# Performance work log

Measured on AMD Instinct MI355X. Metric: run time of the kernel, lower is better.

Reference implementation:

```python
import jax, jax.numpy as jnp
import numpy as np

B, M, H, NH, D, L = 4, 1024, 1024, 8, 128, 1024
E, TOPK, F = 8, 2, 4096
MU, GAMMA = 0.7, 1.0


def _skew(X):
    # shift every row one step right: [B, M, L] -> [B, M, M+L]
    b, m, l = X.shape
    X = jnp.pad(X, ((0, 0), (0, 0), (0, m + 1)))
    X = X.reshape(b, -1)[:, :-m]
    return X.reshape(b, m, m + l)


def _unskew(X):
    # reverse of _skew: [B, M, M+L] -> [B, M, L] (banded diagonal extraction)
    b, m, lt = X.shape
    l = lt - m
    X = jnp.pad(X.reshape(b, -1), ((0, 0), (0, m)))
    X = X.reshape(b, m, m + l + 1)
    return X[:, :, :l]


def _layernorm(x, g, bta):
    mu = jnp.mean(x, axis=-1, keepdims=True)
    var = jnp.mean(jnp.square(x - mu), axis=-1, keepdims=True)
    return (x - mu) * jax.lax.rsqrt(var + 1e-5) * g + bta


def setup_inputs() -> dict:
    key = jax.random.key(0)
    ks = jax.random.split(key, 12)
    s = 0.02
    return {
        'h': jax.random.normal(ks[0], (B, M, H), jnp.float32),
        'h_cache': jax.random.normal(ks[1], (B, L, H), jnp.float32),
        'pos_encoding': jax.random.normal(ks[2], (1, D, L), jnp.float32) * s,
        'momentum': jnp.zeros((B, M, H), jnp.float32),
        'Wq': jax.random.normal(ks[3], (H, H), jnp.float32) * s,
        'Wk': jax.random.normal(ks[4], (H, H), jnp.float32) * s,
        'Wv': jax.random.normal(ks[5], (H, H), jnp.float32) * s,
        'Wo': jax.random.normal(ks[6], (H, H), jnp.float32) * s,
        'gate_w': jax.random.normal(ks[7], (H, E), jnp.float32) * s,
        'gate_b': jnp.zeros((E,), jnp.float32),
        'w1': jax.random.normal(ks[8], (E, H, F), jnp.float32) * s,
        'b1': jnp.zeros((E, F), jnp.float32),
        'w2': jax.random.normal(ks[9], (E, F, H), jnp.float32) * s,
        'b2': jnp.zeros((E, H), jnp.float32),
        'ln1_g': jnp.ones((H,), jnp.float32),
        'ln1_b': jnp.zeros((H,), jnp.float32),
        'ln2_g': jnp.ones((H,), jnp.float32),
        'ln2_b': jnp.zeros((H,), jnp.float32),
    }


def _heads(x):
    b, n, _ = x.shape
    return x.reshape(b, n, NH, D).transpose(0, 2, 1, 3).reshape(b * NH, n, D)


def reference(h, h_cache, pos_encoding, momentum, Wq, Wk, Wv, Wo,
              gate_w, gate_b, w1, b1, w2, b2, ln1_g, ln1_b, ln2_g, ln2_b):
    b, m, hs = h.shape
    # ---- banded relative-position attention (skew trick) ----
    h_all = jnp.concatenate([h_cache, h], axis=1)            # [B, L+M, H]
    q = _heads(h @ Wq)                                        # [B*K, M, D]
    k = _heads(h_all @ Wk)                                    # [B*K, L+M, D]
    v = _heads(h_all @ Wv)                                    # [B*K, L+M, D]
    ctx = jnp.einsum('bmd,bnd->bmn', q, k)                    # [B*K, M, M+L]
    ctx = _unskew(ctx)                                        # [B*K, M, L]
    pos = jnp.einsum('bmd,dl->bml', q, pos_encoding[0])       # [B*K, M, L]
    attn = jax.nn.softmax((ctx + pos) / np.sqrt(hs), axis=-1)
    attn = _skew(attn)                                        # [B*K, M, M+L]
    out = jnp.einsum('bmn,bnd->bmd', attn, v)                 # [B*K, M, D]
    out = out.reshape(b, NH, m, D).transpose(0, 2, 1, 3).reshape(b, m, hs)
    h1 = _layernorm(h + out @ Wo, ln1_g, ln1_b)
    # ---- MoE (naive balanced top-k gate) + momentum residual ----
    x = h1.reshape(-1, hs)                                    # [N, H]
    logits = x @ gate_w + gate_b                              # [N, E]
    topv, topi = jax.lax.top_k(logits, TOPK)
    wgt = jax.nn.softmax(topv, axis=-1)
    dense = jnp.zeros_like(logits).at[jnp.arange(x.shape[0])[:, None], topi].set(wgt)
    moe = jnp.zeros_like(x)
    for e in range(E):
        ye = jax.nn.relu(x @ w1[e] + b1[e]) @ w2[e] + b2[e]
        moe = moe + dense[:, e:e + 1] * ye
    moe = moe.reshape(b, m, hs)
    mom_new = MU * momentum + GAMMA * moe
    h2 = _layernorm(h1 - mom_new, ln2_g, ln2_b)
    return h2, mom_new
```

## Files before the change

### kernel.cpp

```cpp
#include <hip/hip_runtime.h>


typedef short short8 __attribute__((ext_vector_type(8)));
typedef float f32x4 __attribute__((ext_vector_type(4)));

typedef const void __attribute__((address_space(1)))* gas1_t;
typedef void __attribute__((address_space(3)))* las3_t;
#define ASYNC16(G, L) __builtin_amdgcn_global_load_lds((gas1_t)(G), (las3_t)(L), 16, 0, 0)

#define DEV __device__ __forceinline__

DEV float bf2f(unsigned short u) {
  union { unsigned int u; float f; } x; x.u = ((unsigned int)u) << 16; return x.f;
}
DEV unsigned short f2bf(float f) {
  union { float f; unsigned int u; } x; x.f = f;
  unsigned int r = x.u + 0x7fffu + ((x.u >> 16) & 1u);
  return (unsigned short)(r >> 16);
}

struct GemmP {
  const unsigned short* Ah; const unsigned short* Al;
  const unsigned short* Bh; const unsigned short* Bl;
  void* C; void* C2;
  const float* bias;
  const float* xtra;
  const int* idx; const int2* tmap; const int* tn;
  long a_zo, a_zi;
  long b_zo, b_zi, b_y;
  long c_zo, c_zi, c_y, c_x;
  long x_zo, x_zi, x_y;
  long bias_z;
  int lda, ldb, ldc, xld;
  int K, Kc, nx, zdiv, mode, split;
};

template <int SPLIT>
__global__ __launch_bounds__(256) void kGemm(GemmP p) {
  const int t = threadIdx.x;
  const int bx = blockIdx.x, by = blockIdx.y, bz = blockIdx.z;
  const int zo = bz / p.zdiv, zi = bz % p.zdiv;
  const int bxn = bx % p.nx, kc = bx / p.nx;

  long aOff = 0, bOff, cOff;
  long ar0, ar1;
  int e = zi;
  if (p.tmap) {
    if (by >= *p.tn) return;
    int2 tm = p.tmap[by];
    e = tm.x;
    long base = tm.y;
    cOff = base * p.ldc + (long)bxn * p.c_x;
    bOff = (long)e * p.b_zi + (long)bxn * 128L * p.ldb;
    if (p.idx) { ar0 = p.idx[base + (t >> 2)]; ar1 = p.idx[base + 64 + (t >> 2)]; }
    else { ar0 = base + (t >> 2); ar1 = ar0 + 64; }
  } else {
    aOff = (long)zo * p.a_zo + (long)zi * p.a_zi;
    bOff = (long)zo * p.b_zo + (long)zi * p.b_zi + (long)by * p.b_y + (long)bxn * 128L * p.ldb;
    cOff = (long)zo * p.c_zo + (long)zi * p.c_zi + (long)by * p.c_y + (long)bxn * p.c_x;
    ar0 = by * 128 + (t >> 2); ar1 = ar0 + 64;
  }

  const int scol = (((t & 3) ^ ((t >> 3) & 3)) << 3);
  const unsigned short* A0h = p.Ah + aOff + ar0 * (long)p.lda + scol;
  const unsigned short* A1h = p.Ah + aOff + ar1 * (long)p.lda + scol;
  const unsigned short* B0h = p.Bh + bOff + (long)(t >> 2) * p.ldb + scol;
  const unsigned short* B1h = B0h + 64L * p.ldb;
  const unsigned short *A0l = nullptr, *A1l = nullptr, *B0l = nullptr, *B1l = nullptr;
  if (SPLIT) {
    A0l = p.Al + aOff + ar0 * (long)p.lda + scol;
    A1l = p.Al + aOff + ar1 * (long)p.lda + scol;
    B0l = p.Bl + bOff + (long)(t >> 2) * p.ldb + scol;
    B1l = B0l + 64L * p.ldb;
  }

  const int wave = t >> 6;
  const int lane = t & 63;
  const int quad = lane >> 4, l15 = lane & 15;
  const int wr = (wave >> 1) * 64, wc = (wave & 1) * 64;
  const int qs = ((quad ^ ((l15 >> 1) & 3)) << 3);

  f32x4 acc[4][4] = {};
  const int kt0 = (kc * p.Kc) >> 5;
  const int ktN = kt0 + (p.Kc >> 5);

  if constexpr (SPLIT) {
    __shared__ short sAh[4096], sAl[4096], sBh[4096], sBl[4096];
    for (int kt = kt0; kt < ktN; ++kt) {
      const int k0 = kt << 5;
      ASYNC16(A0h + k0, &sAh[wave * 512]);
      ASYNC16(A1h + k0, &sAh[2048 + wave * 512]);
      ASYNC16(B0h + k0, &sBh[wave * 512]);
      ASYNC16(B1h + k0, &sBh[2048 + wave * 512]);
      ASYNC16(A0l + k0, &sAl[wave * 512]);
      ASYNC16(A1l + k0, &sAl[2048 + wave * 512]);
      ASYNC16(B0l + k0, &sBl[wave * 512]);
      ASYNC16(B1l + k0, &sBl[2048 + wave * 512]);
      __syncthreads();
      short8 fa[4], fb[4];
#pragma unroll
      for (int i = 0; i < 4; ++i) {
        fa[i] = *(const short8*)&sAh[(wr + i * 16 + l15) * 32 + qs];
        fb[i] = *(const short8*)&sBh[(wc + i * 16 + l15) * 32 + qs];
      }
#pragma unroll
      for (int bi = 0; bi < 4; ++bi)
#pragma unroll
        for (int bj = 0; bj < 4; ++bj)
          acc[bi][bj] = __builtin_amdgcn_mfma_f32_16x16x32_bf16(fa[bi], fb[bj], acc[bi][bj], 0, 0, 0);
      {
        short8 ga[4], gb[4];
#pragma unroll
        for (int i = 0; i < 4; ++i) {
          ga[i] = *(const short8*)&sAl[(wr + i * 16 + l15) * 32 + qs];
          gb[i] = *(const short8*)&sBl[(wc + i * 16 + l15) * 32 + qs];
        }
#pragma unroll
        for (int bi = 0; bi < 4; ++bi)
#pragma unroll
          for (int bj = 0; bj < 4; ++bj) {
            acc[bi][bj] = __builtin_amdgcn_mfma_f32_16x16x32_bf16(fa[bi], gb[bj], acc[bi][bj], 0, 0, 0);
            acc[bi][bj] = __builtin_amdgcn_mfma_f32_16x16x32_bf16(ga[bi], fb[bj], acc[bi][bj], 0, 0, 0);
          }
      }
      __syncthreads();
    }
  } else {
    __shared__ short sA[2][4096], sB[2][4096];
    int cur = 0;
    {
      const int k0 = kt0 << 5;
      ASYNC16(A0h + k0, &sA[0][wave * 512]);
      ASYNC16(A1h + k0, &sA[0][2048 + wave * 512]);
      ASYNC16(B0h + k0, &sB[0][wave * 512]);
      ASYNC16(B1h + k0, &sB[0][2048 + wave * 512]);
    }
    for (int kt = kt0; kt < ktN; ++kt) {
      if (kt + 1 < ktN) {
        const int k1 = (kt + 1) << 5;
        ASYNC16(A0h + k1, &sA[cur ^ 1][wave * 512]);
        ASYNC16(A1h + k1, &sA[cur ^ 1][2048 + wave * 512]);
        ASYNC16(B0h + k1, &sB[cur ^ 1][wave * 512]);
        ASYNC16(B1h + k1, &sB[cur ^ 1][2048 + wave * 512]);
        asm volatile("s_waitcnt vmcnt(4)" ::: "memory");
      } else {
        asm volatile("s_waitcnt vmcnt(0)" ::: "memory");
      }
      __builtin_amdgcn_s_barrier();
      short8 fa[4], fb[4];
#pragma unroll
      for (int i = 0; i < 4; ++i) {
        fa[i] = *(const short8*)&sA[cur][(wr + i * 16 + l15) * 32 + qs];
        fb[i] = *(const short8*)&sB[cur][(wc + i * 16 + l15) * 32 + qs];
      }
#pragma unroll
      for (int bi = 0; bi < 4; ++bi)
#pragma unroll
        for (int bj = 0; bj < 4; ++bj)
          acc[bi][bj] = __builtin_amdgcn_mfma_f32_16x16x32_bf16(fa[bi], fb[bj], acc[bi][bj], 0, 0, 0);
      __builtin_amdgcn_s_barrier();
      cur ^= 1;
    }
  }

  long xOff = 0;
  if (p.mode == 3) xOff = (long)zo * p.x_zo + (long)zi * p.x_zi + (long)by * p.x_y;
#pragma unroll
  for (int bj = 0; bj < 4; ++bj) {
    const int n_loc = wc + bj * 16 + l15;
    float bv = 0.0f;
    if (p.bias) bv = p.bias[(long)e * p.bias_z + (long)bxn * 128 + n_loc];
#pragma unroll
    for (int bi = 0; bi < 4; ++bi) {
#pragma unroll
      for (int r = 0; r < 4; ++r) {
        const int m_loc = wr + bi * 16 + quad * 4 + r;
        float v = acc[bi][bj][r];
        if (p.mode == 0) {
          ((float*)p.C)[cOff + (long)m_loc * p.ldc + n_loc] = v + bv;
        } else if (p.mode == 1) {
          long a = cOff + (long)m_loc * p.ldc + n_loc;
          unsigned short hv = f2bf(v);
          ((unsigned short*)p.C)[a] = hv;
          ((unsigned short*)p.C2)[a] = f2bf(v - bf2f(hv));
        } else if (p.mode == 2) {
          long a = cOff + (long)n_loc * p.ldc + m_loc;
          unsigned short hv = f2bf(v);
          ((unsigned short*)p.C)[a] = hv;
          ((unsigned short*)p.C2)[a] = f2bf(v - bf2f(hv));
        } else if (p.mode == 3) {
          int l = bxn * 128 + n_loc - m_loc;
          float outv;
          if ((unsigned)l < 1024u)
            outv = (v + p.xtra[xOff + (long)m_loc * p.xld + l]) * 0.03125f;
          else
            outv = -1e30f;
          ((float*)p.C)[cOff + (long)m_loc * p.ldc + n_loc] = outv;
        } else if (p.mode == 4) {
          float rv = v + bv;
          rv = rv > 0.0f ? rv : 0.0f;
          ((unsigned short*)p.C)[cOff + (long)m_loc * p.ldc + n_loc] = f2bf(rv);
        } else {
          float av = v + (kc == 0 ? bv : 0.0f);
          atomicAdd(&((float*)p.C)[cOff + (long)m_loc * p.ldc + n_loc], av);
        }
      }
    }
  }
}

__global__ __launch_bounds__(256) void kConcatSplit(const float* __restrict__ h,
                                                    const float* __restrict__ hc,
                                                    unsigned short* __restrict__ Xh,
                                                    unsigned short* __restrict__ Xl) {
  long i = (((long)blockIdx.x) * 256 + threadIdx.x) * 4;
  long b = i >> 21;
  long rem = i & 2097151;
  const float* s = (rem < 1048576) ? (hc + b * 1048576 + rem) : (h + b * 1048576 + (rem - 1048576));
  f32x4 v = *(const f32x4*)s;
#pragma unroll
  for (int j = 0; j < 4; ++j) {
    float x = v[j];
    unsigned short hi = f2bf(x);
    Xh[i + j] = hi;
    Xl[i + j] = f2bf(x - bf2f(hi));
  }
}

__global__ __launch_bounds__(256) void kTransposeSplit(const float* __restrict__ src, long src_z,
                                                       int R, int C,
                                                       unsigned short* __restrict__ dh,
                                                       unsigned short* __restrict__ dl, long dst_z) {
  __shared__ float tile[32][33];
  const int z = blockIdx.z;
  const float* s = src + (long)z * src_z;
  const int c0 = blockIdx.x * 32, r0 = blockIdx.y * 32;
  const int tx = threadIdx.x & 31, ty = threadIdx.x >> 5;
  for (int i = 0; i < 32; i += 8)
    tile[ty + i][tx] = s[(long)(r0 + ty + i) * C + c0 + tx];
  __syncthreads();
  unsigned short* ph = dh + (long)z * dst_z;
  for (int i = 0; i < 32; i += 8) {
    int c = c0 + ty + i;
    float v = tile[tx][ty + i];
    unsigned short hv = f2bf(v);
    ph[(long)c * R + r0 + tx] = hv;
    if (dl) dl[(long)z * dst_z + (long)c * R + r0 + tx] = f2bf(v - bf2f(hv));
  }
}

__global__ __launch_bounds__(256) void kSplitF(const float* __restrict__ src,
                                               unsigned short* __restrict__ hi,
                                               unsigned short* __restrict__ lo, int n4) {
  int i = blockIdx.x * 256 + threadIdx.x;
  if (i >= n4) return;
  f32x4 v = ((const f32x4*)src)[i];
#pragma unroll
  for (int j = 0; j < 4; ++j) {
    float x = v[j];
    unsigned short h = f2bf(x);
    hi[i * 4 + j] = h;
    lo[i * 4 + j] = f2bf(x - bf2f(h));
  }
}

__global__ __launch_bounds__(256) void kSoftmax(const float* __restrict__ S,
                                                unsigned short* __restrict__ Ph,
                                                unsigned short* __restrict__ Pl) {
  __shared__ float red[4];
  const long r = blockIdx.x;
  const float* s = S + r * 1152;
  const int t = threadIdx.x;
  float v[5];
  float mx = -3e38f;
#pragma unroll
  for (int i = 0; i < 5; ++i) {
    int c = t + i * 256;
    v[i] = (c < 1152) ? s[c] : -3e38f;
    mx = fmaxf(mx, v[i]);
  }
  for (int o = 32; o; o >>= 1) mx = fmaxf(mx, __shfl_xor(mx, o));
  if ((t & 63) == 0) red[t >> 6] = mx;
  __syncthreads();
  mx = fmaxf(fmaxf(red[0], red[1]), fmaxf(red[2], red[3]));
  __syncthreads();
  float e[5]; float sum = 0.f;
#pragma unroll
  for (int i = 0; i < 5; ++i) {
    int c = t + i * 256;
    e[i] = (c < 1152) ? expf(v[i] - mx) : 0.f;
    sum += e[i];
  }
  for (int o = 32; o; o >>= 1) sum += __shfl_xor(sum, o);
  if ((t & 63) == 0) red[t >> 6] = sum;
  __syncthreads();
  sum = red[0] + red[1] + red[2] + red[3];
  const float inv = 1.0f / sum;
#pragma unroll
  for (int i = 0; i < 5; ++i) {
    int c = t + i * 256;
    if (c < 1152) {
      float pv = e[i] * inv;
      unsigned short hv = f2bf(pv);
      Ph[r * 1152 + c] = hv;
      Pl[r * 1152 + c] = f2bf(pv - bf2f(hv));
    }
  }
}

DEV float blockReduceSum(float v, float* red) {
  for (int o = 32; o; o >>= 1) v += __shfl_xor(v, o);
  if ((threadIdx.x & 63) == 0) red[threadIdx.x >> 6] = v;
  __syncthreads();
  v = red[0] + red[1] + red[2] + red[3];
  __syncthreads();
  return v;
}

__global__ __launch_bounds__(256) void kLN1(const float* __restrict__ h, const float* __restrict__ aw,
                                            const float* __restrict__ g, const float* __restrict__ b,
                                            float* __restrict__ h1f, unsigned short* __restrict__ h1h) {
  __shared__ float red[4];
  const long r = blockIdx.x;
  const int t = threadIdx.x;
  float x[4]; float s = 0.f;
#pragma unroll
  for (int i = 0; i < 4; ++i) { int c = t + i * 256; x[i] = h[r * 1024 + c] + aw[r * 1024 + c]; s += x[i]; }
  float mu = blockReduceSum(s, red) * (1.0f / 1024.0f);
  float q = 0.f;
#pragma unroll
  for (int i = 0; i < 4; ++i) { float d = x[i] - mu; q += d * d; }
  float var = blockReduceSum(q, red) * (1.0f / 1024.0f);
  float rstd = 1.0f / sqrtf(var + 1e-5f);
#pragma unroll
  for (int i = 0; i < 4; ++i) {
    int c = t + i * 256;
    float y = (x[i] - mu) * rstd * g[c] + b[c];
    h1f[r * 1024 + c] = y;
    h1h[r * 1024 + c] = f2bf(y);
  }
}

__global__ __launch_bounds__(256) void kLN2(const float* __restrict__ h1f, const float* __restrict__ mom,
                                            const float* __restrict__ g, const float* __restrict__ b,
                                            float* __restrict__ out) {
  __shared__ float red[4];
  const long r = blockIdx.x;
  const int t = threadIdx.x;
  float x[4]; float s = 0.f;
#pragma unroll
  for (int i = 0; i < 4; ++i) { int c = t + i * 256; x[i] = h1f[r * 1024 + c] - mom[r * 1024 + c]; s += x[i]; }
  float mu = blockReduceSum(s, red) * (1.0f / 1024.0f);
  float q = 0.f;
#pragma unroll
  for (int i = 0; i < 4; ++i) { float d = x[i] - mu; q += d * d; }
  float var = blockReduceSum(q, red) * (1.0f / 1024.0f);
  float rstd = 1.0f / sqrtf(var + 1e-5f);
#pragma unroll
  for (int i = 0; i < 4; ++i) {
    int c = t + i * 256;
    out[r * 1024 + c] = (x[i] - mu) * rstd * g[c] + b[c];
  }
}

__global__ __launch_bounds__(256) void kGate(const float* __restrict__ h1f, const float* __restrict__ gw,
                                             const float* __restrict__ gb,
                                             int2* __restrict__ sel, float2* __restrict__ wgt) {
  const int w = threadIdx.x >> 6, lane = threadIdx.x & 63;
  const long r = (long)blockIdx.x * 4 + w;
  float acc[8] = {0, 0, 0, 0, 0, 0, 0, 0};
  const float* xr = h1f + r * 1024;
  for (int kk = lane; kk < 1024; kk += 64) {
    float x = xr[kk];
    const float* gg = gw + kk * 8;
#pragma unroll
    for (int e = 0; e < 8; ++e) acc[e] += x * gg[e];
  }
#pragma unroll
  for (int e = 0; e < 8; ++e)
    for (int o = 32; o; o >>= 1) acc[e] += __shfl_xor(acc[e], o);
  if (lane == 0) {
    float lg[8];
#pragma unroll
    for (int e = 0; e < 8; ++e) lg[e] = acc[e] + gb[e];
    int e0 = 0; float v0 = lg[0];
#pragma unroll
    for (int e = 1; e < 8; ++e) if (lg[e] > v0) { v0 = lg[e]; e0 = e; }
    int e1 = -1; float v1 = -3e38f;
#pragma unroll
    for (int e = 0; e < 8; ++e) if (e != e0 && lg[e] > v1) { v1 = lg[e]; e1 = e; }
    float ed = expf(v1 - v0);
    float si = 1.0f / (1.0f + ed);
    sel[r] = make_int2(e0, e1);
    wgt[r] = make_float2(si, ed * si);
  }
}

__global__ void kCount(const int2* __restrict__ sel, int* __restrict__ cnt) {
  int r = blockIdx.x * 256 + threadIdx.x;
  if (r < 4096) { int2 s = sel[r]; atomicAdd(&cnt[s.x], 1); atomicAdd(&cnt[s.y], 1); }
}
__global__ void kScan(const int* __restrict__ cnt, int* __restrict__ off,
                      int2* __restrict__ tmap, int* __restrict__ tn) {
  if (threadIdx.x == 0) {
    int run = 0, nt = 0;
    for (int e = 0; e < 8; ++e) {
      off[e] = run;
      int nb = (cnt[e] + 127) >> 7;
      for (int j = 0; j < nb; ++j) { tmap[nt] = make_int2(e, run + (j << 7)); ++nt; }
      run += nb << 7;
    }
    *tn = nt;
  }
}
__global__ void kScatter(const int2* __restrict__ sel, const int* __restrict__ off,
                         int* __restrict__ cur, int* __restrict__ bucket, int2* __restrict__ slotof) {
  int r = blockIdx.x * 256 + threadIdx.x;
  if (r < 4096) {
    int2 s = sel[r];
    int a0 = off[s.x] + atomicAdd(&cur[s.x], 1);
    int a1 = off[s.y] + atomicAdd(&cur[s.y], 1);
    bucket[a0] = r; bucket[a1] = r;
    slotof[r] = make_int2(a0, a1);
  }
}

__global__ __launch_bounds__(256) void kCombine(const float* __restrict__ Z, const int2* __restrict__ slotof,
                                                const float2* __restrict__ wgt, const float* __restrict__ mom_in,
                                                float* __restrict__ mom_out) {
  const long r = blockIdx.x;
  const int t = threadIdx.x;
  int2 sl = slotof[r];
  float2 w = wgt[r];
  const float* z0 = Z + (long)sl.x * 1024;
  const float* z1 = Z + (long)sl.y * 1024;
#pragma unroll
  for (int i = 0; i < 4; ++i) {
    int c = t + i * 256;
    float moe = w.x * z0[c] + w.y * z1[c];
    mom_out[r * 1024 + c] = 0.7f * mom_in[r * 1024 + c] + moe;
  }
}

extern "C" void kernel_launch(void* const* d_in, const int* in_sizes, int n_in,
                              void* d_out, int out_size, void* d_ws, size_t ws_size,
                              hipStream_t stream) {
  (void)in_sizes; (void)n_in; (void)out_size; (void)ws_size;
  const float* h       = (const float*)d_in[0];
  const float* h_cache = (const float*)d_in[1];
  const float* pos     = (const float*)d_in[2];
  const float* mom_in  = (const float*)d_in[3];
  const float* Wq      = (const float*)d_in[4];
  const float* Wk      = (const float*)d_in[5];
  const float* Wv      = (const float*)d_in[6];
  const float* Wo      = (const float*)d_in[7];
  const float* gate_w  = (const float*)d_in[8];
  const float* gate_b  = (const float*)d_in[9];
  const float* w1      = (const float*)d_in[10];
  const float* b1      = (const float*)d_in[11];
  const float* w2      = (const float*)d_in[12];
  const float* b2      = (const float*)d_in[13];
  const float* ln1g    = (const float*)d_in[14];
  const float* ln1b    = (const float*)d_in[15];
  const float* ln2g    = (const float*)d_in[16];
  const float* ln2b    = (const float*)d_in[17];
  float* out = (float*)d_out;

  char* ws = (char*)d_ws;
  float*          S     = (float*)(ws + 0L);
  unsigned short* Y1    = (unsigned short*)(ws + 0L);
  unsigned short* Oh    = (unsigned short*)(ws + 0L);
  unsigned short* Ol    = (unsigned short*)(ws + 8388608L);
  float*          Ppos  = (float*)(ws + 75497472L);
  unsigned short* w1T   = (unsigned short*)(ws + 75497472L);
  unsigned short* Ph    = (unsigned short*)(ws + 142606336L);
  unsigned short* Pl    = (unsigned short*)(ws + 180355072L);
  unsigned short* w2T   = (unsigned short*)(ws + 142606336L);
  unsigned short* Xh    = (unsigned short*)(ws + 218103808L);
  unsigned short* Xl    = (unsigned short*)(ws + 234881024L);
  float*          attnO = (float*)(ws + 218103808L);
  float*          attnWo= (float*)(ws + 234881024L);
  unsigned short* kh    = (unsigned short*)(ws + 251658240L);
  unsigned short* kl    = (unsigned short*)(ws + 268435456L);
  float*          h1f   = (float*)(ws + 251658240L);
  unsigned short* h1h   = (unsigned short*)(ws + 268435456L);
  unsigned short* VTh   = (unsigned short*)(ws + 285212672L);
  unsigned short* VTl   = (unsigned short*)(ws + 301989888L);
  unsigned short* qh    = (unsigned short*)(ws + 318767104L);
  unsigned short* ql    = (unsigned short*)(ws + 327155712L);
  float*          qtmp  = (float*)(ws + 335544320L);
  float*          Z     = (float*)(ws + 335544320L);
  unsigned short* WqTh  = (unsigned short*)(ws + 373293056L);
  unsigned short* WqTl  = (unsigned short*)(ws + 375390208L);
  unsigned short* WkTh  = (unsigned short*)(ws + 377487360L);
  unsigned short* WkTl  = (unsigned short*)(ws + 379584512L);
  unsigned short* WvTh  = (unsigned short*)(ws + 381681664L);
  unsigned short* WvTl  = (unsigned short*)(ws + 383778816L);
  unsigned short* WoTh  = (unsigned short*)(ws + 385875968L);
  unsigned short* WoTl  = (unsigned short*)(ws + 387973120L);
  unsigned short* posTh = (unsigned short*)(ws + 390070272L);
  unsigned short* posTl = (unsigned short*)(ws + 390332416L);
  int2*           sel   = (int2*)(ws + 390594560L);
  float2*         wgt   = (float2*)(ws + 390627328L);
  int2*           slotof= (int2*)(ws + 390660096L);
  int*            bucket= (int*)(ws + 390692864L);
  int*            cnt   = (int*)(ws + 390729728L);
  int*            cur   = (int*)(ws + 390729760L);
  int*            off   = (int*)(ws + 390729792L);
  int2*           tmap  = (int2*)(ws + 390729856L);
  int*            tn    = (int*)(ws + 390730496L);

  kConcatSplit<<<8192, 256, 0, stream>>>(h, h_cache, Xh, Xl);
  kTransposeSplit<<<dim3(32, 32, 1), 256, 0, stream>>>(Wq, 0, 1024, 1024, WqTh, WqTl, 0);
  kTransposeSplit<<<dim3(32, 32, 1), 256, 0, stream>>>(Wk, 0, 1024, 1024, WkTh, WkTl, 0);
  kTransposeSplit<<<dim3(32, 32, 1), 256, 0, stream>>>(Wv, 0, 1024, 1024, WvTh, WvTl, 0);
  kTransposeSplit<<<dim3(32, 32, 1), 256, 0, stream>>>(Wo, 0, 1024, 1024, WoTh, WoTl, 0);
  kTransposeSplit<<<dim3(32, 4, 1), 256, 0, stream>>>(pos, 0, 128, 1024, posTh, posTl, 0);

  hipMemsetAsync(qtmp, 0, 16777216L, stream);
  {
    GemmP p{}; p.zdiv = 1; p.split = 1; p.mode = 5;
    p.Ah = Xh + 1048576; p.Al = Xl + 1048576; p.Bh = WqTh; p.Bl = WqTl;
    p.C = qtmp;
    p.lda = 1024; p.ldb = 1024; p.ldc = 1024; p.K = 1024; p.Kc = 512; p.nx = 8;
    p.a_zo = 2097152; p.c_zo = 1048576; p.c_y = 131072; p.c_x = 128;
    kGemm<1><<<dim3(16, 8, 4), 256, 0, stream>>>(p);
  }
  kSplitF<<<4096, 256, 0, stream>>>(qtmp, qh, ql, 1048576);
  {
    GemmP p{}; p.zdiv = 1; p.split = 1; p.mode = 1;
    p.Ah = Xh; p.Al = Xl; p.Bh = WkTh; p.Bl = WkTl;
    p.C = kh; p.C2 = kl;
    p.lda = 1024; p.ldb = 1024; p.ldc = 1024; p.K = 1024; p.Kc = 1024; p.nx = 8;
    p.c_y = 131072; p.c_x = 128;
    kGemm<1><<<dim3(8, 64, 1), 256, 0, stream>>>(p);
  }
  {
    GemmP p{}; p.zdiv = 1; p.split = 1; p.mode = 2;
    p.Ah = Xh; p.Al = Xl; p.Bh = WvTh; p.Bl = WvTl;
    p.C = VTh; p.C2 = VTl;
    p.lda = 1024; p.ldb = 1024; p.ldc = 2048; p.K = 1024; p.Kc = 1024; p.nx = 8;
    p.a_zo = 2097152; p.c_zo = 2097152; p.c_y = 128; p.c_x = 262144;
    kGemm<1><<<dim3(8, 16, 4), 256, 0, stream>>>(p);
  }

  hipMemsetAsync(attnO, 0, 16777216L, stream);
  for (int hf = 0; hf < 2; ++hf) {
    const long qo = hf * 2097152L, ko = hf * 4194304L, vo = hf * 4194304L;
    {
      GemmP p{}; p.zdiv = 8; p.split = 1; p.mode = 0;
      p.Ah = qh + qo; p.Al = ql + qo; p.Bh = posTh; p.Bl = posTl;
      p.C = Ppos;
      p.lda = 1024; p.ldb = 128; p.ldc = 1024; p.K = 128; p.Kc = 128; p.nx = 8;
      p.a_zo = 1048576; p.a_zi = 128;
      p.c_zo = 8388608; p.c_zi = 1048576; p.c_y = 131072; p.c_x = 128;
      kGemm<1><<<dim3(8, 8, 16), 256, 0, stream>>>(p);
    }
    {
      GemmP p{}; p.zdiv = 8; p.split = 1; p.mode = 3;
      p.Ah = qh + qo; p.Al = ql + qo; p.Bh = kh + ko; p.Bl = kl + ko;
      p.C = S; p.xtra = Ppos;
      p.lda = 1024; p.ldb = 1024; p.ldc = 1152; p.xld = 1024; p.K = 128; p.Kc = 128; p.nx = 9;
      p.a_zo = 1048576; p.a_zi = 128;
      p.b_zo = 2097152; p.b_zi = 128; p.b_y = 131072;
      p.c_zo = 9437184; p.c_zi = 1179648; p.c_y = 147456; p.c_x = 128;
      p.x_zo = 8388608; p.x_zi = 1048576; p.x_y = 131072;
      kGemm<1><<<dim3(9, 8, 16), 256, 0, stream>>>(p);
    }
    kSoftmax<<<16384, 256, 0, stream>>>(S, Ph, Pl);
    {
      GemmP p{}; p.zdiv = 8; p.split = 1; p.mode = 5;
      p.Ah = Ph; p.Al = Pl; p.Bh = VTh + vo; p.Bl = VTl + vo;
      p.C = attnO + hf * 2097152L;
      p.lda = 1152; p.ldb = 2048; p.ldc = 1024; p.K = 1152; p.Kc = 384; p.nx = 1;
      p.a_zo = 9437184; p.a_zi = 1179648;
      p.b_zo = 2097152; p.b_zi = 262144; p.b_y = 128;
      p.c_zo = 1048576; p.c_zi = 128; p.c_y = 131072; p.c_x = 128;
      kGemm<1><<<dim3(3, 8, 16), 256, 0, stream>>>(p);
    }
  }

  kSplitF<<<4096, 256, 0, stream>>>(attnO, Oh, Ol, 1048576);
  hipMemsetAsync(attnWo, 0, 16777216L, stream);
  {
    GemmP p{}; p.zdiv = 1; p.split = 1; p.mode = 5;
    p.Ah = Oh; p.Al = Ol; p.Bh = WoTh; p.Bl = WoTl;
    p.C = attnWo;
    p.lda = 1024; p.ldb = 1024; p.ldc = 1024; p.K = 1024; p.Kc = 512; p.nx = 8;
    p.c_y = 131072; p.c_x = 128;
    kGemm<1><<<dim3(16, 32, 1), 256, 0, stream>>>(p);
  }
  kLN1<<<4096, 256, 0, stream>>>(h, attnWo, ln1g, ln1b, h1f, h1h);

  kGate<<<1024, 256, 0, stream>>>(h1f, gate_w, gate_b, sel, wgt);
  hipMemsetAsync(cnt, 0, 64, stream);
  hipMemsetAsync(bucket, 0, 36864, stream);
  kCount<<<16, 256, 0, stream>>>(sel, cnt);
  kScan<<<1, 64, 0, stream>>>(cnt, off, tmap, tn);
  kScatter<<<16, 256, 0, stream>>>(sel, off, cur, bucket, slotof);

  kTransposeSplit<<<dim3(128, 32, 8), 256, 0, stream>>>(w1, 4194304L, 1024, 4096, w1T, nullptr, 4194304L);
  kTransposeSplit<<<dim3(32, 128, 8), 256, 0, stream>>>(w2, 4194304L, 4096, 1024, w2T, nullptr, 4194304L);
  {
    GemmP p{}; p.zdiv = 1; p.split = 0; p.mode = 4;
    p.Ah = h1h; p.Bh = w1T;
    p.C = Y1;
    p.idx = bucket; p.tmap = tmap; p.tn = tn;
    p.bias = b1; p.bias_z = 4096;
    p.lda = 1024; p.ldb = 1024; p.ldc = 4096; p.K = 1024; p.Kc = 1024; p.nx = 32;
    p.b_zi = 4194304; p.c_x = 128;
    kGemm<0><<<dim3(32, 72, 1), 256, 0, stream>>>(p);
  }
  hipMemsetAsync(Z, 0, 37748736L, stream);
  {
    GemmP p{}; p.zdiv = 1; p.split = 0; p.mode = 5;
    p.Ah = Y1; p.Bh = w2T;
    p.C = Z;
    p.tmap = tmap; p.tn = tn;
    p.bias = b2; p.bias_z = 1024;
    p.lda = 4096; p.ldb = 4096; p.ldc = 1024; p.K = 4096; p.Kc = 2048; p.nx = 8;
    p.b_zi = 4194304; p.c_x = 128;
    kGemm<0><<<dim3(16, 72, 1), 256, 0, stream>>>(p);
  }

  float* mom_out = out + 4194304;
  kCombine<<<4096, 256, 0, stream>>>(Z, slotof, wgt, mom_in, mom_out);
  kLN2<<<4096, 256, 0, stream>>>(h1f, mom_out, ln2g, ln2b, out);
}
```

Before: 1.502 ms.

## Add 128x256-tile 512-thread GEMM kernel for MoE expert matmuls

Adds a new kGemmW kernel with 8 waves covering a 128x256 output tile, double-buffered async LDS loads, and uses it for both MoE expert GEMMs (w1 and w2) with halved grid width. The wider tile reuses each A tile across twice as many columns, cutting A-operand global traffic and block count. The original kGemm drops its non-split double-buffered path, so any remaining non-split calls now run single-buffered with full syncs, which may slow them. The larger block also needs more LDS and registers per block, which may lower occupancy.

```diff
diff --git a/kernel.cpp b/kernel.cpp
--- a/kernel.cpp
+++ b/kernel.cpp
@@ -84,83 +84,47 @@
   const int kt0 = (kc * p.Kc) >> 5;
   const int ktN = kt0 + (p.Kc >> 5);
 
-  if constexpr (SPLIT) {
-    __shared__ short sAh[4096], sAl[4096], sBh[4096], sBl[4096];
-    for (int kt = kt0; kt < ktN; ++kt) {
-      const int k0 = kt << 5;
-      ASYNC16(A0h + k0, &sAh[wave * 512]);
-      ASYNC16(A1h + k0, &sAh[2048 + wave * 512]);
-      ASYNC16(B0h + k0, &sBh[wave * 512]);
-      ASYNC16(B1h + k0, &sBh[2048 + wave * 512]);
+  __shared__ short sAh[4096], sAl[4096], sBh[4096], sBl[4096];
+  for (int kt = kt0; kt < ktN; ++kt) {
+    const int k0 = kt << 5;
+    ASYNC16(A0h + k0, &sAh[wave * 512]);
+    ASYNC16(A1h + k0, &sAh[2048 + wave * 512]);
+    ASYNC16(B0h + k0, &sBh[wave * 512]);
+    ASYNC16(B1h + k0, &sBh[2048 + wave * 512]);
+    if (SPLIT) {
       ASYNC16(A0l + k0, &sAl[wave * 512]);
       ASYNC16(A1l + k0, &sAl[2048 + wave * 512]);
       ASYNC16(B0l + k0, &sBl[wave * 512]);
       ASYNC16(B1l + k0, &sBl[2048 + wave * 512]);
-      __syncthreads();
-      short8 fa[4], fb[4];
+    }
+    __syncthreads();
+    short8 fa[4], fb[4];
+#pragma unroll
+    for (int i = 0; i < 4; ++i) {
+      fa[i] = *(const short8*)&sAh[(wr + i * 16 + l15) * 32 + qs];
+      fb[i] = *(const short8*)&sBh[(wc + i * 16 + l15) * 32 + qs];
+    }
+#pragma unroll
+    for (int bi = 0; bi < 4; ++bi)
+#pragma unroll
+      for (int bj = 0; bj < 4; ++bj)
+        acc[bi][bj] = __builtin_amdgcn_mfma_f32_16x16x32_bf16(fa[bi], fb[bj], acc[bi][bj], 0, 0, 0);
+    if (SPLIT) {
+      short8 ga[4], gb[4];
 #pragma unroll
       for (int i = 0; i < 4; ++i) {
-        fa[i] = *(const short8*)&sAh[(wr + i * 16 + l15) * 32 + qs];
-        fb[i] = *(const short8*)&sBh[(wc + i * 16 + l15) * 32 + qs];
+        ga[i] = *(const short8*)&sAl[(wr + i * 16 + l15) * 32 + qs];
+        gb[i] = *(const short8*)&sBl[(wc + i * 16 + l15) * 32 + qs];
       }
 #pragma unroll
       for (int bi = 0; bi < 4; ++bi)
 #pragma unroll
-        for (int bj = 0; bj < 4; ++bj)
-          acc[bi][bj] = __builtin_amdgcn_mfma_f32_16x16x32_bf16(fa[bi], fb[bj], acc[bi][bj], 0, 0, 0);
-      {
-        short8 ga[4], gb[4];
-#pragma unroll
-        for (int i = 0; i < 4; ++i) {
-          ga[i] = *(const short8*)&sAl[(wr + i * 16 + l15) * 32 + qs];
-          gb[i] = *(const short8*)&sBl[(wc + i * 16 + l15) * 32 + qs];
+        for (int bj = 0; bj < 4; ++bj) {
+          acc[bi][bj] = __builtin_amdgcn_mfma_f32_16x16x32_bf16(fa[bi], gb[bj], acc[bi][bj], 0, 0, 0);
+          acc[bi][bj] = __builtin_amdgcn_mfma_f32_16x16x32_bf16(ga[bi], fb[bj], acc[bi][bj], 0, 0, 0);
         }
-#pragma unroll
-        for (int bi = 0; bi < 4; ++bi)
-#pragma unroll
-          for (int bj = 0; bj < 4; ++bj) {
-            acc[bi][bj] = __builtin_amdgcn_mfma_f32_16x16x32_bf16(fa[bi], gb[bj], acc[bi][bj], 0, 0, 0);
-            acc[bi][bj] = __builtin_amdgcn_mfma_f32_16x16x32_bf16(ga[bi], fb[bj], acc[bi][bj], 0, 0, 0);
-          }
-      }
-      __syncthreads();
-    }
-  } else {
-    __shared__ short sA[2][4096], sB[2][4096];
-    int cur = 0;
-    {
-      const int k0 = kt0 << 5;
-      ASYNC16(A0h + k0, &sA[0][wave * 512]);
-      ASYNC16(A1h + k0, &sA[0][2048 + wave * 512]);
-      ASYNC16(B0h + k0, &sB[0][wave * 512]);
-      ASYNC16(B1h + k0, &sB[0][2048 + wave * 512]);
-    }
-    for (int kt = kt0; kt < ktN; ++kt) {
-      if (kt + 1 < ktN) {
-        const int k1 = (kt + 1) << 5;
-        ASYNC16(A0h + k1, &sA[cur ^ 1][wave * 512]);
-        ASYNC16(A1h + k1, &sA[cur ^ 1][2048 + wave * 512]);
-        ASYNC16(B0h + k1, &sB[cur ^ 1][wave * 512]);
-        ASYNC16(B1h + k1, &sB[cur ^ 1][2048 + wave * 512]);
-        asm volatile("s_waitcnt vmcnt(4)" ::: "memory");
-      } else {
-        asm volatile("s_waitcnt vmcnt(0)" ::: "memory");
-      }
-      __builtin_amdgcn_s_barrier();
-      short8 fa[4], fb[4];
-#pragma unroll
-      for (int i = 0; i < 4; ++i) {
-        fa[i] = *(const short8*)&sA[cur][(wr + i * 16 + l15) * 32 + qs];
-        fb[i] = *(const short8*)&sB[cur][(wc + i * 16 + l15) * 32 + qs];
-      }
-#pragma unroll
-      for (int bi = 0; bi < 4; ++bi)
-#pragma unroll
-        for (int bj = 0; bj < 4; ++bj)
-          acc[bi][bj] = __builtin_amdgcn_mfma_f32_16x16x32_bf16(fa[bi], fb[bj], acc[bi][bj], 0, 0, 0);
-      __builtin_amdgcn_s_barrier();
-      cur ^= 1;
-    }
+    }
+    __syncthreads();
   }
 
   long xOff = 0;
@@ -197,6 +161,93 @@
             outv = -1e30f;
           ((float*)p.C)[cOff + (long)m_loc * p.ldc + n_loc] = outv;
         } else if (p.mode == 4) {
+          float rv = v + bv;
+          rv = rv > 0.0f ? rv : 0.0f;
+          ((unsigned short*)p.C)[cOff + (long)m_loc * p.ldc + n_loc] = f2bf(rv);
+        } else {
+          float av = v + (kc == 0 ? bv : 0.0f);
+          atomicAdd(&((float*)p.C)[cOff + (long)m_loc * p.ldc + n_loc], av);
+        }
+      }
+    }
+  }
+}
+
+__global__ __launch_bounds__(512) void kGemmW(GemmP p) {
+  const int t = threadIdx.x;
+  const int bx = blockIdx.x, by = blockIdx.y;
+  const int bxn = bx % p.nx, kc = bx / p.nx;
+  if (by >= *p.tn) return;
+  int2 tm = p.tmap[by];
+  const int e = tm.x;
+  const long base = tm.y;
+  const long cOff = base * p.ldc + (long)bxn * p.c_x;
+  const long bOff = (long)e * p.b_zi + (long)bxn * 256L * p.ldb;
+  long ar0;
+  if (p.idx) ar0 = p.idx[base + (t >> 2)];
+  else       ar0 = base + (t >> 2);
+
+  const int scol = (((t & 3) ^ ((t >> 3) & 3)) << 3);
+  const unsigned short* A0 = p.Ah + ar0 * (long)p.lda + scol;
+  const unsigned short* B0 = p.Bh + bOff + (long)(t >> 2) * p.ldb + scol;
+  const unsigned short* B1 = B0 + 128L * p.ldb;
+
+  __shared__ short sA[2][4096], sB[2][8192];
+  const int wave = t >> 6;
+  const int lane = t & 63;
+  const int quad = lane >> 4, l15 = lane & 15;
+  const int wr = (wave >> 2) * 64;
+  const int wc = (wave & 3) * 64;
+  const int qs = ((quad ^ ((l15 >> 1) & 3)) << 3);
+
+  f32x4 acc[4][4] = {};
+  const int kt0 = (kc * p.Kc) >> 5;
+  const int ktN = kt0 + (p.Kc >> 5);
+  int cur = 0;
+  {
+    const int k0 = kt0 << 5;
+    ASYNC16(A0 + k0, &sA[0][wave * 512]);
+    ASYNC16(B0 + k0, &sB[0][wave * 512]);
+    ASYNC16(B1 + k0, &sB[0][4096 + wave * 512]);
+  }
+  for (int kt = kt0; kt < ktN; ++kt) {
+    if (kt + 1 < ktN) {
+      const int k1 = (kt + 1) << 5;
+      ASYNC16(A0 + k1, &sA[cur ^ 1][wave * 512]);
+      ASYNC16(B0 + k1, &sB[cur ^ 1][wave * 512]);
+      ASYNC16(B1 + k1, &sB[cur ^ 1][4096 + wave * 512]);
+      asm volatile("s_waitcnt vmcnt(3)" ::: "memory");
+    } else {
+      asm volatile("s_waitcnt vmcnt(0)" ::: "memory");
+    }
+    __builtin_amdgcn_s_barrier();
+    short8 fa[4], fb[4];
+#pragma unroll
+    for (int i = 0; i < 4; ++i) {
+      fa[i] = *(const short8*)&sA[cur][(wr + i * 16 + l15) * 32 + qs];
+      fb[i] = *(const short8*)&sB[cur][(wc + i * 16 + l15) * 32 + qs];
+    }
+#pragma unroll
+    for (int bi = 0; bi < 4; ++bi)
+#pragma unroll
+      for (int bj = 0; bj < 4; ++bj)
+        acc[bi][bj] = __builtin_amdgcn_mfma_f32_16x16x32_bf16(fa[bi], fb[bj], acc[bi][bj], 0, 0, 0);
+    __builtin_amdgcn_s_barrier();
+    cur ^= 1;
+  }
+
+#pragma unroll
+  for (int bj = 0; bj < 4; ++bj) {
+    const int n_loc = wc + bj * 16 + l15;
+    float bv = 0.0f;
+    if (p.bias) bv = p.bias[(long)e * p.bias_z + (long)bxn * 256 + n_loc];
+#pragma unroll
+    for (int bi = 0; bi < 4; ++bi) {
+#pragma unroll
+      for (int r = 0; r < 4; ++r) {
+        const int m_loc = wr + bi * 16 + quad * 4 + r;
+        float v = acc[bi][bj][r];
+        if (p.mode == 4) {
           float rv = v + bv;
           rv = rv > 0.0f ? rv : 0.0f;
           ((unsigned short*)p.C)[cOff + (long)m_loc * p.ldc + n_loc] = f2bf(rv);
@@ -607,9 +658,9 @@
     p.C = Y1;
     p.idx = bucket; p.tmap = tmap; p.tn = tn;
     p.bias = b1; p.bias_z = 4096;
-    p.lda = 1024; p.ldb = 1024; p.ldc = 4096; p.K = 1024; p.Kc = 1024; p.nx = 32;
-    p.b_zi = 4194304; p.c_x = 128;
-    kGemm<0><<<dim3(32, 72, 1), 256, 0, stream>>>(p);
+    p.lda = 1024; p.ldb = 1024; p.ldc = 4096; p.K = 1024; p.Kc = 1024; p.nx = 16;
+    p.b_zi = 4194304; p.c_x = 256;
+    kGemmW<<<dim3(16, 72, 1), 512, 0, stream>>>(p);
   }
   hipMemsetAsync(Z, 0, 37748736L, stream);
   {
@@ -618,9 +669,9 @@
     p.C = Z;
     p.tmap = tmap; p.tn = tn;
     p.bias = b2; p.bias_z = 1024;
-    p.lda = 4096; p.ldb = 4096; p.ldc = 1024; p.K = 4096; p.Kc = 2048; p.nx = 8;
-    p.b_zi = 4194304; p.c_x = 128;
-    kGemm<0><<<dim3(16, 72, 1), 256, 0, stream>>>(p);
+    p.lda = 4096; p.ldb = 4096; p.ldc = 1024; p.K = 4096; p.Kc = 2048; p.nx = 4;
+    p.b_zi = 4194304; p.c_x = 256;
+    kGemmW<<<dim3(8, 72, 1), 512, 0, stream>>>(p);
   }
 
   float* mom_out = out + 4194304;
```

Result: faster. 1.467 ms (-2.4%).
